# Kernel optimization log

Measured on AMD Instinct MI355X. Metric: run time of the kernel, lower is better.

## Reference

```python
import jax, jax.numpy as jnp
import numpy as np

H = 512; W = 512; WL = 8; SS = 4; DIM = 128; HEADS = 4; HD = DIM // HEADS; HID = 512
N = WL * WL                      # tokens per window = 64
NW = (H // WL) * (W // WL)       # num windows = 4096
EPS = 1e-5


def _rel_pos_index():
    # standard Swin relative position index for a WLxWL window
    coords = np.stack(np.meshgrid(np.arange(WL), np.arange(WL), indexing='ij')).reshape(2, -1)  # [2, N]
    rel = (coords[:, :, None] - coords[:, None, :]).transpose(1, 2, 0)  # [N, N, 2]
    rel[..., 0] += WL - 1
    rel[..., 1] += WL - 1
    rel[..., 0] *= 2 * WL - 1
    return jnp.asarray(rel.sum(-1))  # [N, N] in [0, (2WL-1)^2)


def _shift_attn_mask():
    # region ids 0/1/2 along each axis per the h_slices/w_slices loop, cnt = 3*h_id + w_id
    ids = np.zeros(H)
    ids[H - WL:H - SS] = 1
    ids[H - SS:] = 2
    img = 3.0 * ids[:, None] + ids[None, :]                     # [H, W]
    wnd = img.reshape(H // WL, WL, W // WL, WL).transpose(0, 2, 1, 3).reshape(NW, N)
    diff = wnd[:, None, :] - wnd[:, :, None]                    # [NW, N, N]
    return jnp.asarray(np.where(diff != 0, -100.0, 0.0).astype(np.float32))


REL_IDX = _rel_pos_index()
ATTN_MASK = _shift_attn_mask()


def _layernorm(v, w, b):
    mu = v.mean(-1, keepdims=True)
    var = v.var(-1, keepdims=True)
    return (v - mu) * jax.lax.rsqrt(var + EPS) * w + b


def setup_inputs() -> dict:
    key = jax.random.key(0)
    ks = jax.random.split(key, 10)
    s = 0.02
    return {
        'x': jax.random.normal(ks[0], (H * W, DIM), dtype=jnp.float32),
        'ln1_w': jnp.ones((DIM,), jnp.float32), 'ln1_b': jnp.zeros((DIM,), jnp.float32),
        'qkv_w': jax.random.normal(ks[1], (3 * DIM, DIM), jnp.float32) * s,
        'qkv_b': jnp.zeros((3 * DIM,), jnp.float32),
        'rel_bias': jax.random.normal(ks[2], ((2 * WL - 1) ** 2, HEADS), jnp.float32) * s,
        'proj_w': jax.random.normal(ks[3], (DIM, DIM), jnp.float32) * s,
        'proj_b': jnp.zeros((DIM,), jnp.float32),
        'ln2_w': jnp.ones((DIM,), jnp.float32), 'ln2_b': jnp.zeros((DIM,), jnp.float32),
        'mlp_w1': jax.random.normal(ks[4], (HID, DIM), jnp.float32) * s,
        'mlp_b1': jnp.zeros((HID,), jnp.float32),
        'mlp_w2': jax.random.normal(ks[5], (DIM, HID), jnp.float32) * s,
        'mlp_b2': jnp.zeros((DIM,), jnp.float32),
    }


def reference(x, ln1_w, ln1_b, qkv_w, qkv_b, rel_bias, proj_w, proj_b,
              ln2_w, ln2_b, mlp_w1, mlp_b1, mlp_w2, mlp_b2):
    skip = x
    xn = _layernorm(x, ln1_w, ln1_b).reshape(H, W, DIM)
    # cyclic shift
    xs = jnp.roll(xn, shift=(-SS, -SS), axis=(0, 1))
    # window partition -> [NW, N, DIM]
    xw = xs.reshape(H // WL, WL, W // WL, WL, DIM).transpose(0, 2, 1, 3, 4).reshape(NW, N, DIM)
    # qkv projection, split heads
    qkv = (xw @ qkv_w.T + qkv_b).reshape(NW, N, 3, HEADS, HD)
    q, k, v = qkv[:, :, 0], qkv[:, :, 1], qkv[:, :, 2]   # each [NW, N, HEADS, HD]
    scale = HD ** -0.5
    scores = jnp.einsum('wnhd,wmhd->whnm', q, k) * scale   # [NW, HEADS, N, N]
    bias = rel_bias[REL_IDX].transpose(2, 0, 1)            # [HEADS, N, N]
    scores = scores + bias[None] + ATTN_MASK[:, None]
    attn = jax.nn.softmax(scores, axis=-1)
    out = jnp.einsum('whnm,wmhd->wnhd', attn, v).reshape(NW, N, DIM)
    out = out @ proj_w.T + proj_b
    # window reverse
    xr = out.reshape(H // WL, W // WL, WL, WL, DIM).transpose(0, 2, 1, 3, 4).reshape(H, W, DIM)
    # reverse cyclic shift
    xr = jnp.roll(xr, shift=(SS, SS), axis=(0, 1)).reshape(H * W, DIM)
    x1 = skip + xr
    # FFN block
    h = _layernorm(x1, ln2_w, ln2_b)
    h = jax.nn.gelu(h @ mlp_w1.T + mlp_b1) @ mlp_w2.T + mlp_b2
    return x1 + h
```

## Files before the change

### kernel.cpp

```cpp
#include <hip/hip_runtime.h>
#include <hip/hip_bf16.h>


typedef __bf16 bf16x8 __attribute__((ext_vector_type(8)));
typedef __bf16 bf16x2 __attribute__((ext_vector_type(2)));
typedef float f32x4 __attribute__((ext_vector_type(4)));

#define MFMA16(a, b, c) __builtin_amdgcn_mfma_f32_16x16x32_bf16(a, b, c, 0, 0, 0)
#define LGKM_BARRIER() do { \
    asm volatile("s_waitcnt lgkmcnt(0)" ::: "memory"); \
    __builtin_amdgcn_s_barrier(); } while (0)

#define SS 4
#define XS 136
#define QKS 40
#define PSS 72

#define QKV_W_OFF 0
#define PROJ_W_OFF 98304
#define W1_OFF 131072
#define W2_OFF 262144
#define BIAS_OFF 393216

__device__ __forceinline__ int regid(int u) { return (u >= 508) ? 2 : ((u >= 504) ? 1 : 0); }

__global__ __launch_bounds__(256) void prep_kernel(
    const float* __restrict__ qkv_w, const float* __restrict__ proj_w,
    const float* __restrict__ w1, const float* __restrict__ w2,
    const float* __restrict__ rel_bias, unsigned char* __restrict__ ws) {
  int tid = blockIdx.x * 256 + threadIdx.x;
  __bf16* qw = (__bf16*)(ws + QKV_W_OFF);
  __bf16* pw = (__bf16*)(ws + PROJ_W_OFF);
  __bf16* w1b = (__bf16*)(ws + W1_OFF);
  __bf16* w2b = (__bf16*)(ws + W2_OFF);
  float* btbl = (float*)(ws + BIAS_OFF);
  if (tid < 49152) {
    int e = tid & 7, lane = (tid >> 3) & 63, kk = (tid >> 9) & 3;
    int f = tid >> 11;
    int h = f / 6, nt = f % 6;
    int j = (nt >> 1) * 128 + h * 32 + (nt & 1) * 16 + (lane & 15);
    int k = kk * 32 + (lane >> 4) * 8 + e;
    qw[tid] = (__bf16)qkv_w[j * 128 + k];
  }
  if (tid < 16384) {
    int e = tid & 7, lane = (tid >> 3) & 63, kk = (tid >> 9) & 3;
    int nt2 = (tid >> 11) & 1, wid = (tid >> 12) & 3;
    int j = wid * 32 + nt2 * 16 + (lane & 15);
    int k = kk * 32 + (lane >> 4) * 8 + e;
    pw[tid] = (__bf16)proj_w[j * 128 + k];
  }
  if (tid < 65536) {
    { int e = tid & 7, lane = (tid >> 3) & 63, kk = (tid >> 9) & 3;
      int nt = (tid >> 11) & 3, wid = (tid >> 13) & 7;
      int j = wid * 64 + nt * 16 + (lane & 15);
      int k = kk * 32 + (lane >> 4) * 8 + e;
      w1b[tid] = (__bf16)w1[j * 128 + k]; }
    { int e = tid & 7, lane = (tid >> 3) & 63, kk = (tid >> 9) & 15, wid = (tid >> 13) & 7;
      int j = wid * 16 + (lane & 15);
      int k = kk * 32 + (lane >> 4) * 8 + e;
      w2b[tid] = (__bf16)w2[j * 512 + k]; }
  }
  if (tid < 16384) {
    int i = tid & 3, lane = (tid >> 2) & 63;
    int kt = (tid >> 8) & 3, qt = (tid >> 10) & 3, h = (tid >> 12) & 3;
    int n = qt * 16 + (lane & 15);
    int m = kt * 16 + (lane >> 4) * 4 + i;
    int idx = ((n >> 3) - (m >> 3) + 7) * 15 + ((n & 7) - (m & 7) + 7);
    btbl[tid] = rel_bias[idx * 4 + h];
  }
}

__global__ __launch_bounds__(256, 2) void attn_kernel(
    const float* __restrict__ x, const float* __restrict__ ln1_w, const float* __restrict__ ln1_b,
    const float* __restrict__ qkv_b, const float* __restrict__ proj_b,
    const unsigned char* __restrict__ ws, float* __restrict__ out) {
  __shared__ __attribute__((aligned(16))) __bf16 xn[64 * XS];
  __shared__ __attribute__((aligned(16))) __bf16 wreg[4][5120];
  __shared__ __attribute__((aligned(16))) __bf16 vt[4][32 * PSS];
  __shared__ __attribute__((aligned(16))) int rid[64];

  const int w = blockIdx.x;
  const int wi = w >> 6, wj = w & 63;
  const int tid = threadIdx.x;
  const int wid = tid >> 6, lane = tid & 63;
  const int lr = lane & 15, lk = lane >> 4;
  const bool edge = (wi == 63) || (wj == 63);
  const f32x4 zero4 = {0.f, 0.f, 0.f, 0.f};

  const __bf16* qw = (const __bf16*)(ws + QKV_W_OFF);
  bf16x8 bw[6][4];
  float qb[6];
#pragma unroll
  for (int nt = 0; nt < 6; nt++) {
    qb[nt] = qkv_b[(nt >> 1) * 128 + wid * 32 + (nt & 1) * 16 + lr];
#pragma unroll
    for (int kk = 0; kk < 4; kk++)
      bw[nt][kk] = *(const bf16x8*)(qw + ((wid * 6 + nt) * 4 + kk) * 512 + lane * 8);
  }

  {
    int n = tid >> 2, q = tid & 3;
    int r = n >> 3, c = n & 7;
    int io = (wi * 8 + r + SS) & 511;
    int jo = (wj * 8 + c + SS) & 511;
    size_t gid = (size_t)io * 512 + jo;
    const float4* xp = (const float4*)(x + gid * 128 + q * 32);
    float4 xv[8];
    float s = 0.f, s2 = 0.f;
#pragma unroll
    for (int t = 0; t < 8; t++) {
      float4 v = xp[t]; xv[t] = v;
      s += v.x + v.y + v.z + v.w;
      s2 += v.x * v.x + v.y * v.y + v.z * v.z + v.w * v.w;
    }
    s += __shfl_xor(s, 1); s += __shfl_xor(s, 2);
    s2 += __shfl_xor(s2, 1); s2 += __shfl_xor(s2, 2);
    float mean = s * (1.f / 128.f);
    float var = s2 * (1.f / 128.f) - mean * mean;
    float rstd = rsqrtf(var + 1e-5f);
    const float4* wv = (const float4*)(ln1_w + q * 32);
    const float4* bv = (const float4*)(ln1_b + q * 32);
    __bf16* dst = xn + n * XS + q * 32;
#pragma unroll
    for (int t = 0; t < 8; t++) {
      float4 wt = wv[t], bt = bv[t], v = xv[t];
      dst[t * 4 + 0] = (__bf16)((v.x - mean) * rstd * wt.x + bt.x);
      dst[t * 4 + 1] = (__bf16)((v.y - mean) * rstd * wt.y + bt.y);
      dst[t * 4 + 2] = (__bf16)((v.z - mean) * rstd * wt.z + bt.z);
      dst[t * 4 + 3] = (__bf16)((v.w - mean) * rstd * wt.w + bt.w);
    }
    if (q == 0) rid[n] = 3 * regid(wi * 8 + r) + regid(wj * 8 + c);
  }
  LGKM_BARRIER();

  {
    const float scale = 0.17677669529663687f;
    __bf16* qbase = &wreg[wid][0];
    __bf16* kbase = &wreg[wid][2560];
    __bf16* vbase = &vt[wid][0];
#pragma unroll
    for (int st = 0; st < 4; st++) {
      bf16x8 a[4];
#pragma unroll
      for (int kk = 0; kk < 4; kk++)
        a[kk] = *(const bf16x8*)(xn + (st * 16 + lr) * XS + kk * 32 + lk * 8);
#pragma unroll
      for (int nt = 0; nt < 6; nt++) {
        f32x4 acc = zero4;
#pragma unroll
        for (int kk = 0; kk < 4; kk++) acc = MFMA16(a[kk], bw[nt][kk], acc);
        float bias = qb[nt];
        int dl = (nt & 1) * 16 + lr;
        if (nt < 2) {
#pragma unroll
          for (int i = 0; i < 4; i++)
            qbase[(st * 16 + lk * 4 + i) * QKS + dl] = (__bf16)((acc[i] + bias) * scale);
        } else if (nt < 4) {
#pragma unroll
          for (int i = 0; i < 4; i++)
            kbase[(st * 16 + lk * 4 + i) * QKS + dl] = (__bf16)(acc[i] + bias);
        } else {
#pragma unroll
          for (int i = 0; i < 4; i++)
            vbase[dl * PSS + st * 16 + lk * 4 + i] = (__bf16)(acc[i] + bias);
        }
      }
    }
  }

  const __bf16* pw = (const __bf16*)(ws + PROJ_W_OFF);
  bf16x8 pwf[2][4];
  float pb2[2];
#pragma unroll
  for (int nt2 = 0; nt2 < 2; nt2++) {
    pb2[nt2] = proj_b[wid * 32 + nt2 * 16 + lr];
#pragma unroll
    for (int kk = 0; kk < 4; kk++)
      pwf[nt2][kk] = *(const bf16x8*)(pw + ((wid * 2 + nt2) * 4 + kk) * 512 + lane * 8);
  }
  const float* btbl = (const float*)(ws + BIAS_OFF);
  f32x4 bc[4][4];
#pragma unroll
  for (int qt = 0; qt < 4; qt++)
#pragma unroll
    for (int kt = 0; kt < 4; kt++)
      bc[qt][kt] = *(const f32x4*)(btbl + ((wid * 4 + qt) * 4 + kt) * 256 + lane * 4);

  int gidx[4][4];
#pragma unroll
  for (int st = 0; st < 4; st++)
#pragma unroll
    for (int i = 0; i < 4; i++) {
      int rr = st * 16 + lk * 4 + i;
      int io = (wi * 8 + (rr >> 3) + SS) & 511;
      int jo = (wj * 8 + (rr & 7) + SS) & 511;
      gidx[st][i] = io * 512 + jo;
    }
  float xres[4][2][4];
#pragma unroll
  for (int st = 0; st < 4; st++)
#pragma unroll
    for (int nt2 = 0; nt2 < 2; nt2++)
#pragma unroll
      for (int i = 0; i < 4; i++)
        xres[st][nt2][i] = x[(size_t)gidx[st][i] * 128 + wid * 32 + nt2 * 16 + lr];

  {
    __bf16* reg0 = &wreg[wid][0];
    bf16x8 kf[4], qf[4], vf[2][2];
#pragma unroll
    for (int kt = 0; kt < 4; kt++)
      kf[kt] = *(const bf16x8*)(reg0 + 2560 + (kt * 16 + lr) * QKS + lk * 8);
#pragma unroll
    for (int qt = 0; qt < 4; qt++)
      qf[qt] = *(const bf16x8*)(reg0 + (qt * 16 + lr) * QKS + lk * 8);
#pragma unroll
    for (int dt = 0; dt < 2; dt++)
#pragma unroll
      for (int kk = 0; kk < 2; kk++)
        vf[dt][kk] = *(const bf16x8*)(&vt[wid][(dt * 16 + lr) * PSS + kk * 32 + lk * 8]);
    asm volatile("s_waitcnt lgkmcnt(0)" ::: "memory");
    __builtin_amdgcn_sched_barrier(0);

    int4 rk[4];
    if (edge) {
#pragma unroll
      for (int kt = 0; kt < 4; kt++) rk[kt] = *(const int4*)&rid[kt * 16 + lk * 4];
    }

#pragma unroll
    for (int qt = 0; qt < 4; qt++) {
      f32x4 s[4];
#pragma unroll
      for (int kt = 0; kt < 4; kt++) s[kt] = MFMA16(kf[kt], qf[qt], bc[qt][kt]);
      if (edge) {
        int rq = rid[qt * 16 + lr];
#pragma unroll
        for (int kt = 0; kt < 4; kt++) {
          s[kt][0] += (rk[kt].x != rq) ? -100.f : 0.f;
          s[kt][1] += (rk[kt].y != rq) ? -100.f : 0.f;
          s[kt][2] += (rk[kt].z != rq) ? -100.f : 0.f;
          s[kt][3] += (rk[kt].w != rq) ? -100.f : 0.f;
        }
      }
      float ex[4][4];
      float sum = 0.f;
#pragma unroll
      for (int kt = 0; kt < 4; kt++) {
#pragma unroll
        for (int i = 0; i < 4; i++) { ex[kt][i] = __expf(s[kt][i]); sum += ex[kt][i]; }
      }
      sum += __shfl_xor(sum, 16);
      sum += __shfl_xor(sum, 32);
      float inv = __builtin_amdgcn_rcpf(sum);
      __bf16* psrow = reg0 + (qt * 16 + lr) * PSS;
#pragma unroll
      for (int kt = 0; kt < 4; kt++) {
        bf16x2 p01 = {(__bf16)(ex[kt][0] * inv), (__bf16)(ex[kt][1] * inv)};
        bf16x2 p23 = {(__bf16)(ex[kt][2] * inv), (__bf16)(ex[kt][3] * inv)};
        *(bf16x2*)(psrow + kt * 16 + lk * 4) = p01;
        *(bf16x2*)(psrow + kt * 16 + lk * 4 + 2) = p23;
      }
#pragma unroll
      for (int dt = 0; dt < 2; dt++) {
        bf16x8 pa0 = *(const bf16x8*)(reg0 + (qt * 16 + lr) * PSS + lk * 8);
        bf16x8 pa1 = *(const bf16x8*)(reg0 + (qt * 16 + lr) * PSS + 32 + lk * 8);
        f32x4 acc = MFMA16(pa0, vf[dt][0], zero4);
        acc = MFMA16(pa1, vf[dt][1], acc);
#pragma unroll
        for (int i = 0; i < 4; i++)
          reg0[qt * 1152 + (lk * 4 + i) * QKS + dt * 16 + lr] = (__bf16)acc[i];
      }
    }
  }
  LGKM_BARRIER();

  {
#pragma unroll
    for (int st = 0; st < 4; st++) {
      bf16x8 ao[4];
#pragma unroll
      for (int kk = 0; kk < 4; kk++)
        ao[kk] = *(const bf16x8*)(&wreg[kk][st * 1152 + lr * QKS + lk * 8]);
#pragma unroll
      for (int nt2 = 0; nt2 < 2; nt2++) {
        f32x4 acc = zero4;
#pragma unroll
        for (int kk = 0; kk < 4; kk++) acc = MFMA16(ao[kk], pwf[nt2][kk], acc);
        int j = wid * 32 + nt2 * 16 + lr;
#pragma unroll
        for (int i = 0; i < 4; i++) {
          size_t off = (size_t)gidx[st][i] * 128 + j;
          out[off] = xres[st][nt2][i] + acc[i] + pb2[nt2];
        }
      }
    }
  }
}

__device__ __forceinline__ float gelu_fast(float x) {
  float u = 0.7978845608028654f * x * (1.f + 0.044715f * x * x);
  float e = __expf(2.f * u);
  float th = 1.f - 2.f * __builtin_amdgcn_rcpf(e + 1.f);
  return 0.5f * x * (1.f + th);
}

__global__ __launch_bounds__(512, 1) void mlp_kernel(
    const float* __restrict__ ln2_w, const float* __restrict__ ln2_b,
    const float* __restrict__ mlp_b1, const float* __restrict__ mlp_b2,
    const unsigned char* __restrict__ ws, float* __restrict__ out) {
  __shared__ __attribute__((aligned(16))) __bf16 xn[64 * 128];
  __shared__ __attribute__((aligned(16))) __bf16 hb[64 * 512];
  const int tid = threadIdx.x;
  const int wid = tid >> 6, lane = tid & 63;
  const int lr = lane & 15, lk = lane >> 4;
  const f32x4 zero4 = {0.f, 0.f, 0.f, 0.f};

  const __bf16* w1r = (const __bf16*)(ws + W1_OFF);
  const __bf16* w2r = (const __bf16*)(ws + W2_OFF);
  bf16x8 w1f[4][4], w2f[16];
#pragma unroll
  for (int nt = 0; nt < 4; nt++)
#pragma unroll
    for (int kk = 0; kk < 4; kk++)
      w1f[nt][kk] = *(const bf16x8*)(w1r + ((wid * 4 + nt) * 4 + kk) * 512 + lane * 8);
#pragma unroll
  for (int kk = 0; kk < 16; kk++)
    w2f[kk] = *(const bf16x8*)(w2r + (wid * 16 + kk) * 512 + lane * 8);
  float b1v[4];
#pragma unroll
  for (int nt = 0; nt < 4; nt++) b1v[nt] = mlp_b1[wid * 64 + nt * 16 + lr];
  float b2v = mlp_b2[wid * 16 + lr];

  const int n = tid >> 3, q = tid & 7;
  float4 xv[4];
  {
    const float4* xp = (const float4*)(out + (size_t)(blockIdx.x * 256 + n) * 128 + q * 16);
#pragma unroll
    for (int t = 0; t < 4; t++) xv[t] = xp[t];
  }

  for (int tt = 0; tt < 4; tt++) {
    const int row0 = (blockIdx.x * 4 + tt) * 64;

    {
      float s = 0.f, s2 = 0.f;
#pragma unroll
      for (int t = 0; t < 4; t++) {
        float4 v = xv[t];
        s += v.x + v.y + v.z + v.w;
        s2 += v.x * v.x + v.y * v.y + v.z * v.z + v.w * v.w;
      }
      s += __shfl_xor(s, 1); s += __shfl_xor(s, 2); s += __shfl_xor(s, 4);
      s2 += __shfl_xor(s2, 1); s2 += __shfl_xor(s2, 2); s2 += __shfl_xor(s2, 4);
      float mean = s * (1.f / 128.f);
      float var = s2 * (1.f / 128.f) - mean * mean;
      float rstd = rsqrtf(var + 1e-5f);
      const float4* wv = (const float4*)(ln2_w + q * 16);
      const float4* bv = (const float4*)(ln2_b + q * 16);
      bf16x8 o[2];
#pragma unroll
      for (int t = 0; t < 4; t++) {
        float4 wt = wv[t], bt = bv[t], v = xv[t];
        o[t >> 1][(t & 1) * 4 + 0] = (__bf16)((v.x - mean) * rstd * wt.x + bt.x);
        o[t >> 1][(t & 1) * 4 + 1] = (__bf16)((v.y - mean) * rstd * wt.y + bt.y);
        o[t >> 1][(t & 1) * 4 + 2] = (__bf16)((v.z - mean) * rstd * wt.z + bt.z);
        o[t >> 1][(t & 1) * 4 + 3] = (__bf16)((v.w - mean) * rstd * wt.w + bt.w);
      }
      *(bf16x8*)(xn + n * 128 + (((q * 2 + 0) ^ (n & 15)) << 3)) = o[0];
      *(bf16x8*)(xn + n * 128 + (((q * 2 + 1) ^ (n & 15)) << 3)) = o[1];
    }
    if (tt < 3) {
      const float4* xp = (const float4*)(out + (size_t)(row0 + 64 + n) * 128 + q * 16);
#pragma unroll
      for (int t = 0; t < 4; t++) xv[t] = xp[t];
    }
    LGKM_BARRIER();

#pragma unroll 1
    for (int st = 0; st < 4; st++) {
      bf16x8 a1[4];
#pragma unroll
      for (int kk = 0; kk < 4; kk++)
        a1[kk] = *(const bf16x8*)(xn + (st * 16 + lr) * 128 + (((kk * 4 + lk) ^ lr) << 3));
#pragma unroll
      for (int nt = 0; nt < 4; nt++) {
        f32x4 acc = zero4;
#pragma unroll
        for (int kk = 0; kk < 4; kk++) acc = MFMA16(a1[kk], w1f[nt][kk], acc);
        int slot = wid * 8 + nt * 2 + (lr >> 3);
#pragma unroll
        for (int i = 0; i < 4; i++) {
          int row = st * 16 + lk * 4 + i;
          hb[row * 512 + ((slot ^ (row & 15)) << 3) + (lr & 7)] =
              (__bf16)gelu_fast(acc[i] + b1v[nt]);
        }
      }
    }
    LGKM_BARRIER();

#pragma unroll 1
    for (int st = 0; st < 4; st++) {
      f32x4 acc0 = zero4, acc1 = zero4;
#pragma unroll
      for (int kk = 0; kk < 8; kk++) {
        bf16x8 a0 = *(const bf16x8*)(hb + (st * 16 + lr) * 512 + (((kk * 4 + lk) ^ lr) << 3));
        bf16x8 a1h = *(const bf16x8*)(hb + (st * 16 + lr) * 512 + ((((kk + 8) * 4 + lk) ^ lr) << 3));
        acc0 = MFMA16(a0, w2f[kk], acc0);
        acc1 = MFMA16(a1h, w2f[kk + 8], acc1);
      }
#pragma unroll
      for (int i = 0; i < 4; i++) {
        size_t off = (size_t)(row0 + st * 16 + lk * 4 + i) * 128 + wid * 16 + lr;
        out[off] = out[off] + acc0[i] + acc1[i] + b2v;
      }
    }
  }
}

extern "C" void kernel_launch(void* const* d_in, const int* in_sizes, int n_in,
                              void* d_out, int out_size, void* d_ws, size_t ws_size,
                              hipStream_t stream) {
  const float* x      = (const float*)d_in[0];
  const float* ln1_w  = (const float*)d_in[1];
  const float* ln1_b  = (const float*)d_in[2];
  const float* qkv_w  = (const float*)d_in[3];
  const float* qkv_b  = (const float*)d_in[4];
  const float* rel_b  = (const float*)d_in[5];
  const float* proj_w = (const float*)d_in[6];
  const float* proj_b = (const float*)d_in[7];
  const float* ln2_w  = (const float*)d_in[8];
  const float* ln2_b  = (const float*)d_in[9];
  const float* mlp_w1 = (const float*)d_in[10];
  const float* mlp_b1 = (const float*)d_in[11];
  const float* mlp_w2 = (const float*)d_in[12];
  const float* mlp_b2 = (const float*)d_in[13];
  float* out = (float*)d_out;
  unsigned char* ws = (unsigned char*)d_ws;

  prep_kernel<<<256, 256, 0, stream>>>(qkv_w, proj_w, mlp_w1, mlp_w2, rel_b, ws);
  attn_kernel<<<4096, 256, 0, stream>>>(x, ln1_w, ln1_b, qkv_b, proj_b, ws, out);
  mlp_kernel<<<1024, 512, 0, stream>>>(ln2_w, ln2_b, mlp_b1, mlp_b2, ws, out);
}
```

Measured before the change: 291.8 us.

## Split MLP hidden dim into two chunks to shrink LDS and raise occupancy

```diff
diff --git a/kernel.cpp b/kernel.cpp
--- a/kernel.cpp
+++ b/kernel.cpp
@@ -50,9 +50,10 @@
     pw[tid] = (__bf16)proj_w[j * 128 + k];
   }
   if (tid < 65536) {
-    { int e = tid & 7, lane = (tid >> 3) & 63, kk = (tid >> 9) & 3;
-      int nt = (tid >> 11) & 3, wid = (tid >> 13) & 7;
-      int j = wid * 64 + nt * 16 + (lane & 15);
+    {
+      int e = tid & 7, lane = (tid >> 3) & 63, kk = (tid >> 9) & 3;
+      int nt = (tid >> 11) & 1, wid = (tid >> 12) & 7, c = (tid >> 15) & 1;
+      int j = c * 256 + wid * 32 + nt * 16 + (lane & 15);
       int k = kk * 32 + (lane >> 4) * 8 + e;
       w1b[tid] = (__bf16)w1[j * 128 + k]; }
     { int e = tid & 7, lane = (tid >> 3) & 63, kk = (tid >> 9) & 15, wid = (tid >> 13) & 7;
@@ -298,19 +299,17 @@
   }
 }
 
-__device__ __forceinline__ float gelu_fast(float x) {
-  float u = 0.7978845608028654f * x * (1.f + 0.044715f * x * x);
-  float e = __expf(2.f * u);
-  float th = 1.f - 2.f * __builtin_amdgcn_rcpf(e + 1.f);
-  return 0.5f * x * (1.f + th);
+__device__ __forceinline__ float gelu_sig(float x) {
+  float e = exp2f(x * -2.4554826f);
+  return x * __builtin_amdgcn_rcpf(1.f + e);
 }
 
-__global__ __launch_bounds__(512, 1) void mlp_kernel(
+__global__ __launch_bounds__(512, 4) void mlp_kernel(
     const float* __restrict__ ln2_w, const float* __restrict__ ln2_b,
     const float* __restrict__ mlp_b1, const float* __restrict__ mlp_b2,
     const unsigned char* __restrict__ ws, float* __restrict__ out) {
   __shared__ __attribute__((aligned(16))) __bf16 xn[64 * 128];
-  __shared__ __attribute__((aligned(16))) __bf16 hb[64 * 512];
+  __shared__ __attribute__((aligned(16))) __bf16 hb[64 * 256];
   const int tid = threadIdx.x;
   const int wid = tid >> 6, lane = tid & 63;
   const int lr = lane & 15, lk = lane >> 4;
@@ -318,36 +317,30 @@
 
   const __bf16* w1r = (const __bf16*)(ws + W1_OFF);
   const __bf16* w2r = (const __bf16*)(ws + W2_OFF);
-  bf16x8 w1f[4][4], w2f[16];
-#pragma unroll
-  for (int nt = 0; nt < 4; nt++)
-#pragma unroll
-    for (int kk = 0; kk < 4; kk++)
-      w1f[nt][kk] = *(const bf16x8*)(w1r + ((wid * 4 + nt) * 4 + kk) * 512 + lane * 8);
+
+  bf16x8 w2f[16];
 #pragma unroll
   for (int kk = 0; kk < 16; kk++)
     w2f[kk] = *(const bf16x8*)(w2r + (wid * 16 + kk) * 512 + lane * 8);
-  float b1v[4];
-#pragma unroll
-  for (int nt = 0; nt < 4; nt++) b1v[nt] = mlp_b1[wid * 64 + nt * 16 + lr];
+  float b1v[2][2];
+#pragma unroll
+  for (int c = 0; c < 2; c++)
+#pragma unroll
+    for (int nt = 0; nt < 2; nt++)
+      b1v[c][nt] = mlp_b1[c * 256 + wid * 32 + nt * 16 + lr];
   float b2v = mlp_b2[wid * 16 + lr];
-
-  const int n = tid >> 3, q = tid & 7;
-  float4 xv[4];
-  {
-    const float4* xp = (const float4*)(out + (size_t)(blockIdx.x * 256 + n) * 128 + q * 16);
-#pragma unroll
-    for (int t = 0; t < 4; t++) xv[t] = xp[t];
-  }
 
   for (int tt = 0; tt < 4; tt++) {
     const int row0 = (blockIdx.x * 4 + tt) * 64;
 
     {
+      int n = tid >> 3, q = tid & 7;
+      const float4* xp = (const float4*)(out + (size_t)(row0 + n) * 128 + q * 16);
+      float4 xv[4];
       float s = 0.f, s2 = 0.f;
 #pragma unroll
       for (int t = 0; t < 4; t++) {
-        float4 v = xv[t];
+        float4 v = xp[t]; xv[t] = v;
         s += v.x + v.y + v.z + v.w;
         s2 += v.x * v.x + v.y * v.y + v.z * v.z + v.w * v.w;
       }
@@ -370,51 +363,59 @@
       *(bf16x8*)(xn + n * 128 + (((q * 2 + 0) ^ (n & 15)) << 3)) = o[0];
       *(bf16x8*)(xn + n * 128 + (((q * 2 + 1) ^ (n & 15)) << 3)) = o[1];
     }
-    if (tt < 3) {
-      const float4* xp = (const float4*)(out + (size_t)(row0 + 64 + n) * 128 + q * 16);
-#pragma unroll
-      for (int t = 0; t < 4; t++) xv[t] = xp[t];
-    }
-    LGKM_BARRIER();
+    __syncthreads();
+
+    f32x4 macc[4] = {zero4, zero4, zero4, zero4};
 
 #pragma unroll 1
-    for (int st = 0; st < 4; st++) {
-      bf16x8 a1[4];
-#pragma unroll
-      for (int kk = 0; kk < 4; kk++)
-        a1[kk] = *(const bf16x8*)(xn + (st * 16 + lr) * 128 + (((kk * 4 + lk) ^ lr) << 3));
-#pragma unroll
-      for (int nt = 0; nt < 4; nt++) {
-        f32x4 acc = zero4;
-#pragma unroll
-        for (int kk = 0; kk < 4; kk++) acc = MFMA16(a1[kk], w1f[nt][kk], acc);
-        int slot = wid * 8 + nt * 2 + (lr >> 3);
-#pragma unroll
-        for (int i = 0; i < 4; i++) {
-          int row = st * 16 + lk * 4 + i;
-          hb[row * 512 + ((slot ^ (row & 15)) << 3) + (lr & 7)] =
-              (__bf16)gelu_fast(acc[i] + b1v[nt]);
+    for (int c = 0; c < 2; c++) {
+      bf16x8 w1f[2][4];
+#pragma unroll
+      for (int nt = 0; nt < 2; nt++)
+#pragma unroll
+        for (int kk = 0; kk < 4; kk++)
+          w1f[nt][kk] = *(const bf16x8*)(w1r + (((c * 8 + wid) * 2 + nt) * 4 + kk) * 512 + lane * 8);
+
+#pragma unroll
+      for (int st = 0; st < 4; st++) {
+        bf16x8 a1[4];
+#pragma unroll
+        for (int kk = 0; kk < 4; kk++)
+          a1[kk] = *(const bf16x8*)(xn + (st * 16 + lr) * 128 + (((kk * 4 + lk) ^ lr) << 3));
+#pragma unroll
+        for (int nt = 0; nt < 2; nt++) {
+          f32x4 acc = zero4;
+#pragma unroll
+          for (int kk = 0; kk < 4; kk++) acc = MFMA16(a1[kk], w1f[nt][kk], acc);
+          int slot = wid * 4 + nt * 2 + (lr >> 3);
+#pragma unroll
+          for (int i = 0; i < 4; i++) {
+            int row = st * 16 + lk * 4 + i;
+            hb[row * 256 + ((slot ^ (row & 15)) << 3) + (lr & 7)] =
+                (__bf16)gelu_sig(acc[i] + b1v[c][nt]);
+          }
         }
       }
-    }
-    LGKM_BARRIER();
-
-#pragma unroll 1
-    for (int st = 0; st < 4; st++) {
-      f32x4 acc0 = zero4, acc1 = zero4;
-#pragma unroll
-      for (int kk = 0; kk < 8; kk++) {
-        bf16x8 a0 = *(const bf16x8*)(hb + (st * 16 + lr) * 512 + (((kk * 4 + lk) ^ lr) << 3));
-        bf16x8 a1h = *(const bf16x8*)(hb + (st * 16 + lr) * 512 + ((((kk + 8) * 4 + lk) ^ lr) << 3));
-        acc0 = MFMA16(a0, w2f[kk], acc0);
-        acc1 = MFMA16(a1h, w2f[kk + 8], acc1);
-      }
+      __syncthreads();
+
+#pragma unroll
+      for (int st = 0; st < 4; st++) {
+#pragma unroll
+        for (int kks = 0; kks < 8; kks++) {
+          bf16x8 ah = *(const bf16x8*)(hb + (st * 16 + lr) * 256 + (((kks * 4 + lk) ^ lr) << 3));
+          macc[st] = MFMA16(ah, w2f[c * 8 + kks], macc[st]);
+        }
+      }
+      if (c == 0) __syncthreads();
+    }
+
+#pragma unroll
+    for (int st = 0; st < 4; st++)
 #pragma unroll
       for (int i = 0; i < 4; i++) {
         size_t off = (size_t)(row0 + st * 16 + lk * 4 + i) * 128 + wid * 16 + lr;
-        out[off] = out[off] + acc0[i] + acc1[i] + b2v;
-      }
-    }
+        out[off] = out[off] + macc[st][i] + b2v;
+      }
   }
 }
 
```

Result: slower. 385.4 us (+32.1%).
